# Kernel tuning notes

Hardware: AMD Instinct MI355X
Metric: run time of the kernel (lower is better)

Reference implementation:

```python
import jax, jax.numpy as jnp
import numpy as np

N_NODES = 100_000
N_EDGES = 1_600_000
IN_FEATS = 64
H_DIMS = 64
OUT_A = 2
OUT_B = 21
N_LAYERS = 2
EPS = 1e-5


def setup_inputs() -> dict:
    key = jax.random.key(0)
    ks = jax.random.split(key, 16)
    d = H_DIMS

    def rn(k, shape, scale=0.05):
        return jax.random.normal(k, shape, dtype=jnp.float32) * scale

    return {
        "v": jax.random.normal(ks[0], (N_NODES, IN_FEATS), dtype=jnp.float32),
        "src": jax.random.randint(ks[1], (N_EDGES,), 0, N_NODES),
        "dst": jax.random.randint(ks[2], (N_EDGES,), 0, N_NODES),
        "rel_type": jax.random.randint(ks[3], (N_EDGES,), 0, 3),
        "norm": jax.random.uniform(ks[4], (N_EDGES,), dtype=jnp.float32),
        "emb_W": rn(ks[5], (d, IN_FEATS)),
        "emb_b": jnp.zeros((d,), jnp.float32),
        "emb_gamma": jnp.ones((d,), jnp.float32),
        "emb_beta": jnp.zeros((d,), jnp.float32),
        "rel_weight": rn(ks[6], (3, d, d)),
        "gru_Wih": rn(ks[7], (3 * d, d)),
        "gru_Whh": rn(ks[8], (3 * d, d)),
        "gru_bih": jnp.zeros((3 * d,), jnp.float32),
        "gru_bhh": jnp.zeros((3 * d,), jnp.float32),
        "ker_gamma": jnp.ones((d,), jnp.float32),
        "ker_beta": jnp.zeros((d,), jnp.float32),
        "a_W1": rn(ks[9], (d, d)), "a_b1": jnp.zeros((d,), jnp.float32),
        "a_gamma": jnp.ones((d,), jnp.float32), "a_beta": jnp.zeros((d,), jnp.float32),
        "a_W2": rn(ks[10], (OUT_A, d)), "a_b2": jnp.zeros((OUT_A,), jnp.float32),
        "b_W1": rn(ks[11], (d, d)), "b_b1": jnp.zeros((d,), jnp.float32),
        "b_gamma": jnp.ones((d,), jnp.float32), "b_beta": jnp.zeros((d,), jnp.float32),
        "b_W2": rn(ks[12], (OUT_B, d)), "b_b2": jnp.zeros((OUT_B,), jnp.float32),
    }


def _bn(x, gamma, beta):
    # BatchNorm1d in training mode: batch statistics, biased variance
    mu = jnp.mean(x, axis=0)
    var = jnp.var(x, axis=0)
    return (x - mu) * jax.lax.rsqrt(var + EPS) * gamma + beta


def _gru_cell(x, h, Wih, Whh, bih, bhh):
    # torch nn.GRU single layer, gate order (r, z, n)
    gi = x @ Wih.T + bih
    gh = h @ Whh.T + bhh
    ir, iz, inn = jnp.split(gi, 3, axis=-1)
    hr, hz, hn = jnp.split(gh, 3, axis=-1)
    r = jax.nn.sigmoid(ir + hr)
    z = jax.nn.sigmoid(iz + hz)
    n = jnp.tanh(inn + r * hn)
    return (1.0 - z) * n + z * h


def reference(v, src, dst, rel_type, norm, emb_W, emb_b, emb_gamma, emb_beta,
              rel_weight, gru_Wih, gru_Whh, gru_bih, gru_bhh, ker_gamma, ker_beta,
              a_W1, a_b1, a_gamma, a_beta, a_W2, a_b2,
              b_W1, b_b1, b_gamma, b_beta, b_W2, b_b2):
    # Embedding: Linear -> BN -> ReLU
    h0 = jax.nn.relu(_bn(v @ emb_W.T + emb_b, emb_gamma, emb_beta))
    output = h0
    h = jnp.zeros_like(h0)
    n_nodes = v.shape[0]
    for _ in range(N_LAYERS):
        # per-node relational transform for all 3 relations: [N, 3, d]
        x3 = jnp.einsum('nd,rdk->nrk', output, rel_weight)
        msg = x3[src, rel_type] * norm[:, None]                     # [E, d]
        swh = jax.ops.segment_sum(msg, dst, num_segments=n_nodes)   # [N, d]
        h = _gru_cell(swh, h, gru_Wih, gru_Whh, gru_bih, gru_bhh)
        output = h
    hk = _bn(output, ker_gamma, ker_beta)
    # task heads: Linear -> BN -> ReLU -> Linear (MLP with h_layers=2)
    xa = jax.nn.relu(_bn(hk @ a_W1.T + a_b1, a_gamma, a_beta)) @ a_W2.T + a_b2
    xb = jax.nn.relu(_bn(hk @ b_W1.T + b_b1, b_gamma, b_beta)) @ b_W2.T + b_b2
    return xa, xb
```

## Files before the change

kernel.cpp:

```cpp
#include <hip/hip_runtime.h>

#define NN 100000
#define NE 1600000
#define NP 100096
#define NBKT 391
#define CAP 6144
#define EPSV 1e-5f

typedef unsigned int u32;
typedef unsigned short u16;
typedef unsigned long long u64;
typedef __bf16 bf16x8 __attribute__((ext_vector_type(8)));
typedef float f32x4 __attribute__((ext_vector_type(4)));

#define GLBP(x) ((const __attribute__((address_space(1))) u32*)(x))
#define LDSP(x) ((__attribute__((address_space(3))) u32*)(x))

__device__ __forceinline__ u16 f2bf(float f) {
  u32 x = __float_as_uint(f);
  return (u16)((x + 0x7FFFu + ((x >> 16) & 1u)) >> 16);
}
__device__ __forceinline__ float bf2f(u16 h) { return __uint_as_float(((u32)h) << 16); }
__device__ __forceinline__ u32 pk2(float a, float b) {
  return (u32)f2bf(a) | ((u32)f2bf(b) << 16);
}

__device__ __forceinline__ void pack_one(const float* W, u32* out, int K, int KOT, int i) {
  int q = i & 3, lane = (i >> 2) & 63, f = i >> 8;
  int ks = f / KOT, ot = f - ks * KOT;
  int o = ot * 16 + (lane & 15);
  int k = ks * 32 + (lane >> 4) * 8 + q * 2;
  out[i] = pk2(W[o * K + k], W[o * K + k + 1]);
}

__global__ void setupA(const float* __restrict__ relw, const float* __restrict__ Wih,
                       const float* __restrict__ embW, const float* __restrict__ Whh,
                       float* __restrict__ Wrow, u32* __restrict__ PWem, u32* __restrict__ PWhh) {
  int b = blockIdx.x;
  if (b < 144) {
    int t = b * 256 + threadIdx.x;
    if (t >= 192 * 192) return;
    int kg = t / 192, j = t % 192;
    const float* a = relw + (j >> 6) * 4096 + (j & 63) * 64;
    const float* w = Wih + kg * 64;
    float s = 0.f;
#pragma unroll
    for (int k = 0; k < 64; ++k) s += a[k] * w[k];
    Wrow[kg * 192 + j] = s;
  } else if (b < 152) {
    pack_one(embW, PWem, 64, 4, (b - 144) * 256 + threadIdx.x);
  } else {
    pack_one(Whh, PWhh, 64, 12, (b - 152) * 256 + threadIdx.x);
  }
}

__global__ void pack_wf(const float* __restrict__ Wrow, u32* __restrict__ PWf) {
  pack_one(Wrow, PWf, 192, 12, blockIdx.x * 256 + threadIdx.x);
}

__global__ void fold_pack(const float* __restrict__ Wa, const float* __restrict__ Wb,
                          const float* __restrict__ kacc, const float* __restrict__ kg,
                          u32* __restrict__ P) {
  int i = blockIdx.x * 256 + threadIdx.x;
  int q = i & 3, lane = (i >> 2) & 63, f = i >> 8;
  int ks = f >> 3, ot = f & 7;
  int o = ot * 16 + (lane & 15);
  int k = ks * 32 + (lane >> 4) * 8 + q * 2;
  const float* W = (o < 64) ? (Wa + o * 64) : (Wb + (o - 64) * 64);
  const float inv = 1.f / NN;
  float m0 = kacc[k] * inv;
  float s0 = kg[k] * rsqrtf(kacc[64 + k] * inv - m0 * m0 + EPSV);
  float m1 = kacc[k + 1] * inv;
  float s1 = kg[k + 1] * rsqrtf(kacc[64 + k + 1] * inv - m1 * m1 + EPSV);
  P[i] = pk2(W[k] * s0, W[k + 1] * s1);
}

__global__ __launch_bounds__(256) void countplace(const int* __restrict__ src,
                                                  const int* __restrict__ dst,
                                                  const int* __restrict__ rt,
                                                  const float* __restrict__ nrm,
                                                  int* __restrict__ gcnt,
                                                  u64* __restrict__ region) {
  __shared__ u32 hist[NBKT], gbase[NBKT];
  const int t = threadIdx.x;
  for (int i = t; i < NBKT; i += 256) hist[i] = 0;
  __syncthreads();
  const int e0 = blockIdx.x * 2048 + t;
  u32 rlo[8], rhi[8], lrank[8];
  int bkt[8];
#pragma unroll
  for (int i = 0; i < 8; ++i) {
    int e = e0 + i * 256;
    bkt[i] = -1;
    if (e < NE) {
      int d = dst[e];
      int b = d >> 8;
      bkt[i] = b;
      lrank[i] = atomicAdd(&hist[b], 1u);
      rlo[i] = (u32)src[e] | ((u32)rt[e] << 20) | ((u32)(d & 255) << 22);
      rhi[i] = __float_as_uint(nrm[e]);
    }
  }
  __syncthreads();
  for (int i = t; i < NBKT; i += 256) {
    u32 h = hist[i];
    gbase[i] = h ? (u32)atomicAdd(&gcnt[i], (int)h) : 0u;
  }
  __syncthreads();
#pragma unroll
  for (int i = 0; i < 8; ++i) {
    if (bkt[i] >= 0) {
      u32 pos = gbase[bkt[i]] + lrank[i];
      if (pos < CAP)
        region[(size_t)bkt[i] * CAP + pos] = (u64)rlo[i] | ((u64)rhi[i] << 32);
    }
  }
}

__global__ __launch_bounds__(512) void bucketscan(const int* __restrict__ gcnt,
                                                  int* __restrict__ bbase) {
  int t = threadIdx.x;
  int v = (t < NBKT) ? (gcnt[t] + 768) : 0;
  __shared__ int sh[512];
  sh[t] = v;
  __syncthreads();
#pragma unroll
  for (int off = 1; off < 512; off <<= 1) {
    int u = (t >= off) ? sh[t - off] : 0;
    __syncthreads();
    sh[t] += u;
    __syncthreads();
  }
  if (t < NBKT) bbase[t] = sh[t] - v;
}

__global__ __launch_bounds__(256) void localsort(const int* __restrict__ gcnt,
                                                 const int* __restrict__ bbase,
                                                 const u64* __restrict__ region,
                                                 u64* __restrict__ csr,
                                                 int* __restrict__ rowpr) {
  const int b = blockIdx.x, t = threadIdx.x;
  int n = gcnt[b];
  if (n > CAP) n = CAP;
  const int base = bbase[b];
  __shared__ u32 hist[1024], sc[256];
#pragma unroll
  for (int i = 0; i < 4; ++i) hist[t + 256 * i] = 0;
  __syncthreads();
  for (int i = t; i < n; i += 256)
    atomicAdd(&hist[(u32)(region[(size_t)b * CAP + i] >> 20) & 1023u], 1u);
  __syncthreads();
  u32 a0 = hist[4 * t], a1 = hist[4 * t + 1], a2 = hist[4 * t + 2];
  u32 p0 = (a0 + 1) & ~1u, p1 = (a1 + 1) & ~1u, p2 = (a2 + 1) & ~1u;
  u32 part = p0 + p1 + p2;
  sc[t] = part;
  __syncthreads();
#pragma unroll
  for (int off = 1; off < 256; off <<= 1) {
    u32 u = (t >= off) ? sc[t - off] : 0;
    __syncthreads();
    sc[t] += u;
    __syncthreads();
  }
  u32 ex = sc[t] - part;
  int node = b * 256 + t;
  rowpr[4 * node + 0] = base + (int)ex;
  rowpr[4 * node + 1] = base + (int)(ex + p0);
  rowpr[4 * node + 2] = base + (int)(ex + p0 + p1);
  rowpr[4 * node + 3] = base + (int)(ex + p0 + p1 + p2);
  __syncthreads();
  hist[4 * t + 0] = ex;
  hist[4 * t + 1] = ex + p0;
  hist[4 * t + 2] = ex + p0 + p1;
  __syncthreads();
  for (int i = t; i < n; i += 256) {
    u64 rec = region[(size_t)b * CAP + i];
    u32 pos = atomicAdd(&hist[(u32)(rec >> 20) & 1023u], 1u);
    csr[(size_t)base + pos] = rec;
  }
  __syncthreads();
  if (a0 & 1) csr[(size_t)base + ex + a0] = 0ull;
  if (a1 & 1) csr[(size_t)base + ex + p0 + a1] = 0ull;
  if (a2 & 1) csr[(size_t)base + ex + p0 + p1 + a2] = 0ull;
}

__global__ __launch_bounds__(256) void csr_gather(const int* __restrict__ rowpr,
                                                  const u64* __restrict__ csr,
                                                  const u16* __restrict__ Xbf,
                                                  u16* __restrict__ ACCbf) {
  int wv = blockIdx.x * 4 + (threadIdx.x >> 6);
  int lane = threadIdx.x & 63;
  if (wv >= NN) return;
  const int half = lane >> 5, c2 = lane & 31;
  int4 rp = *reinterpret_cast<const int4*>(rowpr + 4 * wv);
  const int b0 = __builtin_amdgcn_readfirstlane(rp.x);
  const int b1 = __builtin_amdgcn_readfirstlane(rp.y);
  const int b2 = __builtin_amdgcn_readfirstlane(rp.z);
  const int b3 = __builtin_amdgcn_readfirstlane(rp.w);
  const u32* X4 = (const u32*)Xbf;
  float a0x = 0.f, a0y = 0.f, a1x = 0.f, a1y = 0.f, a2x = 0.f, a2y = 0.f;
#define PAIRB(J, AX, AY)                                                        \
  { u32 sA = (u32)__builtin_amdgcn_readlane((int)lo, (J));                      \
    u32 sB = (u32)__builtin_amdgcn_readlane((int)lo, (J) + 1);                  \
    u32 nA = (u32)__builtin_amdgcn_readlane((int)hi, (J));                      \
    u32 nB = (u32)__builtin_amdgcn_readlane((int)hi, (J) + 1);                  \
    u32 srp = half ? sB : sA;                                                   \
    float nm = __uint_as_float(half ? nB : nA);                                 \
    u32 xw = X4[((srp & 0xFFFFFu) << 5) | (u32)c2];                             \
    AX = fmaf(__uint_as_float(xw << 16), nm, AX);                               \
    AY = fmaf(__uint_as_float(xw & 0xFFFF0000u), nm, AY); }
  for (int c = b0; c < b3; c += 64) {
    int m = b3 - c; m = m > 64 ? 64 : m;
    u32 lo = 0, hi = 0;
    if (lane < m) {
      u64 rec = csr[(size_t)c + lane];
      lo = (u32)rec; hi = (u32)(rec >> 32);
    }
    int j1 = b1 - c; j1 = j1 < 0 ? 0 : (j1 > m ? m : j1);
    int j2 = b2 - c; j2 = j2 < 0 ? 0 : (j2 > m ? m : j2);
    int j = 0;
    for (; j + 4 <= j1; j += 4) { PAIRB(j, a0x, a0y) PAIRB(j + 2, a0x, a0y) }
    if (j < j1) { PAIRB(j, a0x, a0y) j += 2; }
    for (; j + 4 <= j2; j += 4) { PAIRB(j, a1x, a1y) PAIRB(j + 2, a1x, a1y) }
    if (j < j2) { PAIRB(j, a1x, a1y) j += 2; }
    for (; j + 4 <= m; j += 4) { PAIRB(j, a2x, a2y) PAIRB(j + 2, a2x, a2y) }
    if (j < m) { PAIRB(j, a2x, a2y) j += 2; }
  }
#undef PAIRB
  a0x += __shfl_xor(a0x, 32); a0y += __shfl_xor(a0y, 32);
  a1x += __shfl_xor(a1x, 32); a1y += __shfl_xor(a1y, 32);
  a2x += __shfl_xor(a2x, 32); a2y += __shfl_xor(a2y, 32);
  if (half == 0) {
    u32* orow = (u32*)(ACCbf + (size_t)wv * 192);
    orow[c2]      = pk2(a0x, a0y);
    orow[32 + c2] = pk2(a1x, a1y);
    orow[64 + c2] = pk2(a2x, a2y);
  }
}

template<int K, int KO, int AF32, int GRU, int CS, int OUTBF>
__global__ __launch_bounds__(512) void gemm_mfma(
    const void* __restrict__ Av, const u32* __restrict__ Wpk, void* __restrict__ Yv,
    const float* __restrict__ bih, const float* __restrict__ bhh,
    const u16* __restrict__ G2B, const u16* __restrict__ Hv,
    float* __restrict__ csum, int n) {
  constexpr int KOT = KO / 16, KS = K / 32;
  constexpr int NFRAG = KS * KOT;
  __shared__ u32 bsh[NFRAG * 256];
  __shared__ float cs[2 * KO];
  const int lane = threadIdx.x & 63, w = threadIdx.x >> 6;
  const int rr = lane & 15, kg = lane >> 4;
  const long mbase = (long)blockIdx.x * 256 + w * 32;
  const u16* Abf = (const u16*)Av;
  const float* Af = (const float*)Av;

  bf16x8 abf[KS][2];
  float4 araw[AF32 ? KS : 1][2][2];
  if (AF32) {
#pragma unroll
    for (int ks = 0; ks < KS; ++ks)
#pragma unroll
      for (int hh = 0; hh < 2; ++hh) {
        long r = mbase + hh * 16 + rr;
        if (r > n - 1) r = n - 1;
        const float* pp = Af + r * K + ks * 32 + kg * 8;
        araw[ks][hh][0] = *(const float4*)pp;
        araw[ks][hh][1] = *(const float4*)(pp + 4);
      }
  } else {
#pragma unroll
    for (int ks = 0; ks < KS; ++ks)
#pragma unroll
      for (int hh = 0; hh < 2; ++hh)
        abf[ks][hh] = *reinterpret_cast<const bf16x8*>(
            Abf + (mbase + hh * 16 + rr) * K + ks * 32 + kg * 8);
  }

  constexpr int PASSES = NFRAG / 8;
#pragma unroll
  for (int i = 0; i < PASSES; ++i) {
    int c = i * 8 + w;
    __builtin_amdgcn_global_load_lds(GLBP(Wpk + (long)c * 256 + lane * 4),
                                     LDSP(&bsh[c * 256]), 16, 0, 0);
  }
  __syncthreads();

  if (AF32) {
#pragma unroll
    for (int ks = 0; ks < KS; ++ks)
#pragma unroll
      for (int hh = 0; hh < 2; ++hh) {
        float4 u0 = araw[ks][hh][0], u1 = araw[ks][hh][1];
        bf16x8 o_;
        o_[0] = __builtin_bit_cast(__bf16, f2bf(u0.x));
        o_[1] = __builtin_bit_cast(__bf16, f2bf(u0.y));
        o_[2] = __builtin_bit_cast(__bf16, f2bf(u0.z));
        o_[3] = __builtin_bit_cast(__bf16, f2bf(u0.w));
        o_[4] = __builtin_bit_cast(__bf16, f2bf(u1.x));
        o_[5] = __builtin_bit_cast(__bf16, f2bf(u1.y));
        o_[6] = __builtin_bit_cast(__bf16, f2bf(u1.z));
        o_[7] = __builtin_bit_cast(__bf16, f2bf(u1.w));
        abf[ks][hh] = o_;
      }
  }

  f32x4 acc[2][KOT] = {};
#pragma unroll
  for (int ks = 0; ks < KS; ++ks) {
#pragma unroll
    for (int o = 0; o < KOT; ++o) {
      bf16x8 bfr = *reinterpret_cast<const bf16x8*>(&bsh[((ks * KOT + o) * 64 + lane) * 4]);
      acc[0][o] = __builtin_amdgcn_mfma_f32_16x16x32_bf16(abf[ks][0], bfr, acc[0][o], 0, 0, 0);
      acc[1][o] = __builtin_amdgcn_mfma_f32_16x16x32_bf16(abf[ks][1], bfr, acc[1][o], 0, 0, 0);
    }
  }

  float s[KOT] = {}, ss[KOT] = {};
  if (GRU == 0) {
#pragma unroll
    for (int tl = 0; tl < 2; ++tl)
#pragma unroll
      for (int o = 0; o < KOT; ++o)
#pragma unroll
        for (int q = 0; q < 4; ++q) {
          long row = mbase + tl * 16 + kg * 4 + q;
          float vv = acc[tl][o][q];
          if (row < n) {
            long off = row * KO + o * 16 + rr;
            if (OUTBF) ((u16*)Yv)[off] = f2bf(vv);
            else       ((float*)Yv)[off] = vv;
            if (CS) { s[o] += vv; ss[o] += vv * vv; }
          }
        }
  } else {
    float bi[12], bh_[12];
#pragma unroll
    for (int g = 0; g < 3; ++g)
#pragma unroll
      for (int o = 0; o < 4; ++o) {
        bi[g * 4 + o] = bih[g * 64 + o * 16 + rr];
        bh_[g * 4 + o] = bhh[g * 64 + o * 16 + rr];
      }
#pragma unroll
    for (int tl = 0; tl < 2; ++tl)
#pragma unroll
      for (int o = 0; o < 4; ++o) {
        int c = o * 16 + rr;
#pragma unroll
        for (int q = 0; q < 4; ++q) {
          long row = mbase + tl * 16 + kg * 4 + q;
          float ir = acc[tl][o][q] + bi[o];
          float iz = acc[tl][o + 4][q] + bi[4 + o];
          float in_ = acc[tl][o + 8][q] + bi[8 + o];
          float hr = bh_[o], hz = bh_[4 + o], hn = bh_[8 + o], hv = 0.f;
          if (GRU == 2) {
            const u16* g2 = G2B + row * 192;
            hr += bf2f(g2[c]); hz += bf2f(g2[64 + c]); hn += bf2f(g2[128 + c]);
            hv = bf2f(Hv[row * 64 + c]);
          }
          float rg = 1.f / (1.f + __expf(-(ir + hr)));
          float zg = 1.f / (1.f + __expf(-(iz + hz)));
          float ng = tanhf(in_ + rg * hn);
          float h = (1.f - zg) * ng + (GRU == 2 ? zg * hv : 0.f);
          if (row < n) {
            ((u16*)Yv)[row * 64 + c] = f2bf(h);
            if (CS) { s[o] += h; ss[o] += h * h; }
          }
        }
      }
  }
  if (CS) {
    constexpr int LIM = (GRU == 0) ? 2 * KO : 128;
    constexpr int CKO = (GRU == 0) ? KO : 64;
    constexpr int OL = (GRU == 0) ? KOT : 4;
    for (int i = threadIdx.x; i < LIM; i += 512) cs[i] = 0.f;
    __syncthreads();
#pragma unroll
    for (int o = 0; o < OL; ++o) {
      int c = o * 16 + rr;
      atomicAdd(&cs[c], s[o]);
      atomicAdd(&cs[CKO + c], ss[o]);
    }
    __syncthreads();
    for (int i = threadIdx.x; i < LIM; i += 512) atomicAdd(&csum[i], cs[i]);
  }
}

__global__ __launch_bounds__(256) void bn_apply_bf(const float* __restrict__ X,
                                                   u16* __restrict__ Y,
                                                   const float* __restrict__ accs,
                                                   const float* __restrict__ gamma,
                                                   const float* __restrict__ beta, int relu) {
  __shared__ float scsh[128];
  int t = threadIdx.x;
  if (t < 64) {
    float mean = accs[t] * (1.f / NN);
    float var = accs[64 + t] * (1.f / NN) - mean * mean;
    float sc = gamma[t] * rsqrtf(var + EPSV);
    scsh[t] = sc;
    scsh[64 + t] = beta[t] - mean * sc;
  }
  __syncthreads();
  long i = (long)blockIdx.x * 256 + t;
  float4 v = reinterpret_cast<const float4*>(X)[i];
  int c = (int)((i * 4) & 63);
  v.x = fmaf(v.x, scsh[c],     scsh[64 + c]);
  v.y = fmaf(v.y, scsh[c + 1], scsh[65 + c]);
  v.z = fmaf(v.z, scsh[c + 2], scsh[66 + c]);
  v.w = fmaf(v.w, scsh[c + 3], scsh[67 + c]);
  if (relu) {
    v.x = fmaxf(v.x, 0.f); v.y = fmaxf(v.y, 0.f);
    v.z = fmaxf(v.z, 0.f); v.w = fmaxf(v.w, 0.f);
  }
  reinterpret_cast<ushort4*>(Y)[i] = make_ushort4(f2bf(v.x), f2bf(v.y), f2bf(v.z), f2bf(v.w));
}

template<int KO>
__global__ __launch_bounds__(256) void headfin_bn(const u16* __restrict__ Z,
                                                  const float* __restrict__ asum,
                                                  const float* __restrict__ asq,
                                                  const float* __restrict__ gamma,
                                                  const float* __restrict__ beta,
                                                  const float* __restrict__ W2,
                                                  const float* __restrict__ b2,
                                                  float* __restrict__ out, int n) {
  __shared__ float ws[KO * 64];
  __shared__ float scsh[128];
  int t = threadIdx.x;
  if (t < 64) {
    float mean = asum[t] * (1.f / NN);
    float var = asq[t] * (1.f / NN) - mean * mean;
    float sc = gamma[t] * rsqrtf(var + EPSV);
    scsh[t] = sc;
    scsh[64 + t] = beta[t] - mean * sc;
  }
  for (int i = t; i < KO * 64; i += 256) ws[i] = W2[i];
  __syncthreads();
  long node = (long)blockIdx.x * 256 + t;
  if (node >= n) return;
  const u16* zr = Z + node * 128;
  float x[64];
#pragma unroll
  for (int i = 0; i < 16; ++i) {
    ushort4 z4 = reinterpret_cast<const ushort4*>(zr)[i];
    int c = i * 4;
    x[c]     = fmaxf(fmaf(bf2f(z4.x), scsh[c],     scsh[64 + c]), 0.f);
    x[c + 1] = fmaxf(fmaf(bf2f(z4.y), scsh[c + 1], scsh[65 + c]), 0.f);
    x[c + 2] = fmaxf(fmaf(bf2f(z4.z), scsh[c + 2], scsh[66 + c]), 0.f);
    x[c + 3] = fmaxf(fmaf(bf2f(z4.w), scsh[c + 3], scsh[67 + c]), 0.f);
  }
#pragma unroll
  for (int o = 0; o < KO; ++o) {
    float a = b2[o];
#pragma unroll
    for (int d = 0; d < 64; ++d) a = fmaf(x[d], ws[o * 64 + d], a);
    out[node * KO + o] = a;
  }
}

extern "C" void kernel_launch(void* const* d_in, const int* in_sizes, int n_in,
                              void* d_out, int out_size, void* d_ws, size_t ws_size,
                              hipStream_t stream) {
  const float* v     = (const float*)d_in[0];
  const int*   src   = (const int*)d_in[1];
  const int*   dst   = (const int*)d_in[2];
  const int*   rt    = (const int*)d_in[3];
  const float* norm  = (const float*)d_in[4];
  const float* emb_W = (const float*)d_in[5];
  const float* emb_g  = (const float*)d_in[7];
  const float* emb_be = (const float*)d_in[8];
  const float* rel_w  = (const float*)d_in[9];
  const float* Wih    = (const float*)d_in[10];
  const float* Whh    = (const float*)d_in[11];
  const float* bih    = (const float*)d_in[12];
  const float* bhh    = (const float*)d_in[13];
  const float* ker_g  = (const float*)d_in[14];
  const float* aW1    = (const float*)d_in[16];
  const float* a_g  = (const float*)d_in[18];
  const float* a_be = (const float*)d_in[19];
  const float* aW2  = (const float*)d_in[20];
  const float* ab2  = (const float*)d_in[21];
  const float* bW1  = (const float*)d_in[22];
  const float* b_g  = (const float*)d_in[24];
  const float* b_be = (const float*)d_in[25];
  const float* bW2  = (const float*)d_in[26];
  const float* bb2  = (const float*)d_in[27];
  float* out = (float*)d_out;

  char* p = (char*)d_ws;
  auto nxt = [&](size_t bytes) -> char* {
    char* r = p; p += (bytes + 255) & ~(size_t)255; return r;
  };
  int*   GCNT = (int*)nxt(512 * 4);
  float* ACCs = (float*)nxt(512 * 4);
  float* Z    = (float*)nxt((size_t)NP * 64 * 4);
  u16*   X1   = (u16*)nxt((size_t)NP * 64 * 2);
  u16*   X2   = (u16*)nxt((size_t)NP * 64 * 2);
  u16*   ACCB = (u16*)nxt((size_t)NP * 192 * 2);
  u16*   G2B  = (u16*)nxt((size_t)NP * 192 * 2);
  u64*   REG  = (u64*)nxt((size_t)NBKT * CAP * 8);
  u64*   CSR  = (u64*)nxt((size_t)(NE + NBKT * 768 + 64) * 8);
  int*   BBAS = (int*)nxt(512 * 4);
  int*   ROWPR = (int*)nxt((size_t)(NP + 8) * 4 * 4);
  u32*   PWf  = (u32*)nxt(18432 * 4);
  u32*   PWem = (u32*)nxt(2048 * 4);
  u32*   PWhh = (u32*)nxt(6144 * 4);
  u32*   PWab = (u32*)nxt(4096 * 4);
  float* WROW = (float*)nxt(147456);

  hipMemsetAsync(GCNT, 0, 1024 * 4, stream);

  setupA<<<176, 256, 0, stream>>>(rel_w, Wih, emb_W, Whh, WROW, PWem, PWhh);
  countplace<<<782, 256, 0, stream>>>(src, dst, rt, norm, GCNT, REG);
  bucketscan<<<1, 512, 0, stream>>>(GCNT, BBAS);
  localsort<<<NBKT, 256, 0, stream>>>(GCNT, BBAS, REG, CSR, ROWPR);
  pack_wf<<<72, 256, 0, stream>>>(WROW, PWf);

  gemm_mfma<64, 64, 1, 0, 1, 0><<<391, 512, 0, stream>>>(v, PWem, Z, nullptr, nullptr,
                                                         nullptr, nullptr, ACCs + 0, NN);
  bn_apply_bf<<<6250, 256, 0, stream>>>(Z, X2, ACCs + 0, emb_g, emb_be, 1);

  csr_gather<<<25000, 256, 0, stream>>>(ROWPR, CSR, X2, ACCB);
  gemm_mfma<192, 192, 0, 1, 0, 1><<<391, 512, 0, stream>>>(ACCB, PWf, X1, bih, bhh,
                                                           nullptr, nullptr, nullptr, NN);

  csr_gather<<<25000, 256, 0, stream>>>(ROWPR, CSR, X1, ACCB);
  gemm_mfma<64, 192, 0, 0, 0, 1><<<391, 512, 0, stream>>>(X1, PWhh, G2B, nullptr, nullptr,
                                                          nullptr, nullptr, nullptr, NN);
  gemm_mfma<192, 192, 0, 2, 1, 1><<<391, 512, 0, stream>>>(ACCB, PWf, X1, bih, bhh,
                                                           G2B, X1, ACCs + 128, NN);

  fold_pack<<<16, 256, 0, stream>>>(aW1, bW1, ACCs + 128, ker_g, PWab);
  gemm_mfma<64, 128, 0, 0, 1, 1><<<391, 512, 0, stream>>>(X1, PWab, ACCB, nullptr, nullptr,
                                                          nullptr, nullptr, ACCs + 256, NN);
  headfin_bn<2><<<391, 256, 0, stream>>>((const u16*)ACCB, ACCs + 256, ACCs + 384,
                                         a_g, a_be, aW2, ab2, out, NN);
  headfin_bn<21><<<391, 256, 0, stream>>>((const u16*)ACCB + 64, ACCs + 320, ACCs + 448,
                                          b_g, b_be, bW2, bb2, out + (long)NN * 2, NN);
}
```

Before: 365.7 us.

## Split fused GRU GEMM into per-gate GEMM blocks plus separate combine kernel

Replaces the monolithic GRU GEMM kernels, which computed all 192 gate outputs per block and applied the nonlinearity in the epilogue, with a gate_gemm that launches one grid slice per gate (r, z, n_input, and n_hidden in layer 2). Layer 2 concatenates the Whh term into the K dimension for the r and z gates. A separate elementwise gru_combine kernel then applies the sigmoid/tanh update and accumulates BN statistics. The aim is more parallel blocks, lower register pressure and less LDS per block, and removal of the separate Whh GEMM. The cost is an extra bf16 round-trip of gate pre-activations through global memory, an extra kernel launch per layer, and bf16 rounding of the pre-activations. Workspace buffers are aliased to make room for the gate outputs.

```diff
diff --git a/kernel.cpp b/kernel.cpp
--- a/kernel.cpp
+++ b/kernel.cpp
@@ -24,6 +24,7 @@
 __device__ __forceinline__ u32 pk2(float a, float b) {
   return (u32)f2bf(a) | ((u32)f2bf(b) << 16);
 }
+__device__ __forceinline__ float sigm(float x) { return 1.f / (1.f + __expf(-x)); }
 
 __device__ __forceinline__ void pack_one(const float* W, u32* out, int K, int KOT, int i) {
   int q = i & 3, lane = (i >> 2) & 63, f = i >> 8;
@@ -34,8 +35,8 @@
 }
 
 __global__ void setupA(const float* __restrict__ relw, const float* __restrict__ Wih,
-                       const float* __restrict__ embW, const float* __restrict__ Whh,
-                       float* __restrict__ Wrow, u32* __restrict__ PWem, u32* __restrict__ PWhh) {
+                       const float* __restrict__ embW,
+                       float* __restrict__ Wrow, u32* __restrict__ PWem) {
   int b = blockIdx.x;
   if (b < 144) {
     int t = b * 256 + threadIdx.x;
@@ -47,15 +48,43 @@
 #pragma unroll
     for (int k = 0; k < 64; ++k) s += a[k] * w[k];
     Wrow[kg * 192 + j] = s;
-  } else if (b < 152) {
+  } else {
     pack_one(embW, PWem, 64, 4, (b - 144) * 256 + threadIdx.x);
+  }
+}
+
+__global__ void pack_g1(const float* __restrict__ Wrow, u32* __restrict__ P) {
+  int i = blockIdx.x * 256 + threadIdx.x;
+  int q = i & 3, lane = (i >> 2) & 63, f = i >> 8;
+  int g = f / 24, fl = f - g * 24;
+  int ks = fl >> 2, o = fl & 3;
+  int row = g * 64 + o * 16 + (lane & 15);
+  int k = ks * 32 + (lane >> 4) * 8 + q * 2;
+  P[i] = pk2(Wrow[row * 192 + k], Wrow[row * 192 + k + 1]);
+}
+
+__global__ void pack_g2(const float* __restrict__ Wrow, const float* __restrict__ Whh,
+                        u32* __restrict__ P) {
+  int i = blockIdx.x * 256 + threadIdx.x;
+  int q = i & 3, lane = (i >> 2) & 63, f = i >> 8;
+  int g = f >> 5, fl = f & 31;
+  int ks = fl >> 2, o = fl & 3;
+  u32 val = 0u;
+  if (ks < 6) {
+    if (g < 3) {
+      int row = g * 64 + o * 16 + (lane & 15);
+      int k = ks * 32 + (lane >> 4) * 8 + q * 2;
+      val = pk2(Wrow[row * 192 + k], Wrow[row * 192 + k + 1]);
+    }
   } else {
-    pack_one(Whh, PWhh, 64, 12, (b - 152) * 256 + threadIdx.x);
-  }
-}
-
-__global__ void pack_wf(const float* __restrict__ Wrow, u32* __restrict__ PWf) {
-  pack_one(Wrow, PWf, 192, 12, blockIdx.x * 256 + threadIdx.x);
+    int g2 = (g < 2) ? g : (g == 3 ? 2 : -1);
+    if (g2 >= 0) {
+      int row = g2 * 64 + o * 16 + (lane & 15);
+      int k = (ks - 6) * 32 + (lane >> 4) * 8 + q * 2;
+      val = pk2(Whh[row * 64 + k], Whh[row * 64 + k + 1]);
+    }
+  }
+  P[i] = val;
 }
 
 __global__ void fold_pack(const float* __restrict__ Wa, const float* __restrict__ Wb,
@@ -238,11 +267,124 @@
   }
 }
 
-template<int K, int KO, int AF32, int GRU, int CS, int OUTBF>
+template<int LAYER>
+__global__ __launch_bounds__(512, 6) void gate_gemm(
+    const u16* __restrict__ A1, const u16* __restrict__ A2,
+    const u32* __restrict__ Pg, u16* __restrict__ GG, int n) {
+  constexpr int KSP = (LAYER == 1) ? 6 : 8;
+  constexpr int NFRAG = KSP * 4;
+  __shared__ u32 bsh[NFRAG * 256];
+  const int g = blockIdx.x / NBKT, blk = blockIdx.x - g * NBKT;
+  int ksl = 0, ksh = 6;
+  if (LAYER == 2) { ksl = (g == 3) ? 6 : 0; ksh = (g == 2) ? 6 : 8; }
+  const int lane = threadIdx.x & 63, w = threadIdx.x >> 6;
+  const int rr = lane & 15, kg = lane >> 4;
+  const long mbase = (long)blk * 256 + w * 32;
+
+  const u32* P = Pg + (long)g * NFRAG * 256;
+#pragma unroll
+  for (int i = 0; i < NFRAG / 8; ++i) {
+    int c = i * 8 + w;
+    __builtin_amdgcn_global_load_lds(GLBP(P + (long)c * 256 + lane * 4),
+                                     LDSP(&bsh[c * 256]), 16, 0, 0);
+  }
+  __syncthreads();
+
+  f32x4 acc[2][4] = {};
+  for (int ks = ksl; ks < ksh; ++ks) {
+    bf16x8 a0, a1;
+    if (ks < 6) {
+      a0 = *reinterpret_cast<const bf16x8*>(A1 + (mbase + rr) * 192 + ks * 32 + kg * 8);
+      a1 = *reinterpret_cast<const bf16x8*>(A1 + (mbase + 16 + rr) * 192 + ks * 32 + kg * 8);
+    } else {
+      a0 = *reinterpret_cast<const bf16x8*>(A2 + (mbase + rr) * 64 + (ks - 6) * 32 + kg * 8);
+      a1 = *reinterpret_cast<const bf16x8*>(A2 + (mbase + 16 + rr) * 64 + (ks - 6) * 32 + kg * 8);
+    }
+#pragma unroll
+    for (int o = 0; o < 4; ++o) {
+      bf16x8 b = *reinterpret_cast<const bf16x8*>(&bsh[((ks * 4 + o) * 64 + lane) * 4]);
+      acc[0][o] = __builtin_amdgcn_mfma_f32_16x16x32_bf16(a0, b, acc[0][o], 0, 0, 0);
+      acc[1][o] = __builtin_amdgcn_mfma_f32_16x16x32_bf16(a1, b, acc[1][o], 0, 0, 0);
+    }
+  }
+
+  u16* Gg = GG + (long)g * ((long)NP * 64);
+#pragma unroll
+  for (int tl = 0; tl < 2; ++tl)
+#pragma unroll
+    for (int o = 0; o < 4; ++o)
+#pragma unroll
+      for (int q = 0; q < 4; ++q) {
+        long row = mbase + tl * 16 + kg * 4 + q;
+        if (row < n) Gg[row * 64 + o * 16 + rr] = f2bf(acc[tl][o][q]);
+      }
+}
+
+template<int USE_H, int CS>
+__global__ __launch_bounds__(256) void gru_combine(
+    const u16* __restrict__ GG, const u16* __restrict__ Hin, u16* __restrict__ Hout,
+    const float* __restrict__ bih, const float* __restrict__ bhh,
+    float* __restrict__ csum) {
+  __shared__ float cs[128];
+  const int t = threadIdx.x;
+  if (CS) {
+    for (int i = t; i < 128; i += 256) cs[i] = 0.f;
+    __syncthreads();
+  }
+  float s[4] = {0.f, 0.f, 0.f, 0.f}, ss[4] = {0.f, 0.f, 0.f, 0.f};
+  const long tot = (long)NN * 16;
+  int c0 = -1;
+  for (long i = (long)blockIdx.x * 256 + t; i < tot; i += (long)gridDim.x * 256) {
+    long node = i >> 4;
+    c0 = (int)(i & 15) * 4;
+    ushort4 vr = *reinterpret_cast<const ushort4*>(GG + node * 64 + c0);
+    ushort4 vz = *reinterpret_cast<const ushort4*>(GG + (long)NP * 64 + node * 64 + c0);
+    ushort4 vi = *reinterpret_cast<const ushort4*>(GG + (long)2 * NP * 64 + node * 64 + c0);
+    ushort4 vh = make_ushort4(0, 0, 0, 0), hv = make_ushort4(0, 0, 0, 0);
+    if (USE_H) {
+      vh = *reinterpret_cast<const ushort4*>(GG + (long)3 * NP * 64 + node * 64 + c0);
+      hv = *reinterpret_cast<const ushort4*>(Hin + node * 64 + c0);
+    }
+    u16 gr[4] = {vr.x, vr.y, vr.z, vr.w};
+    u16 gz[4] = {vz.x, vz.y, vz.z, vz.w};
+    u16 gi[4] = {vi.x, vi.y, vi.z, vi.w};
+    u16 gh[4] = {vh.x, vh.y, vh.z, vh.w};
+    u16 hl[4] = {hv.x, hv.y, hv.z, hv.w};
+    u16 ov[4];
+#pragma unroll
+    for (int k = 0; k < 4; ++k) {
+      int c = c0 + k;
+      float r = sigm(bf2f(gr[k]) + bih[c] + bhh[c]);
+      float z = sigm(bf2f(gz[k]) + bih[64 + c] + bhh[64 + c]);
+      float h;
+      if (USE_H) {
+        float ng = tanhf(bf2f(gi[k]) + bih[128 + c] + r * (bf2f(gh[k]) + bhh[128 + c]));
+        h = (1.f - z) * ng + z * bf2f(hl[k]);
+      } else {
+        float ng = tanhf(bf2f(gi[k]) + bih[128 + c] + r * bhh[128 + c]);
+        h = (1.f - z) * ng;
+      }
+      ov[k] = f2bf(h);
+      if (CS) { s[k] += h; ss[k] += h * h; }
+    }
+    *reinterpret_cast<ushort4*>(Hout + node * 64 + c0) = make_ushort4(ov[0], ov[1], ov[2], ov[3]);
+  }
+  if (CS) {
+    if (c0 >= 0) {
+#pragma unroll
+      for (int k = 0; k < 4; ++k) {
+        atomicAdd(&cs[c0 + k], s[k]);
+        atomicAdd(&cs[64 + c0 + k], ss[k]);
+      }
+    }
+    __syncthreads();
+    if (t < 128) atomicAdd(&csum[t], cs[t]);
+  }
+}
+
+template<int K, int KO, int AF32, int CS, int OUTBF>
 __global__ __launch_bounds__(512) void gemm_mfma(
     const void* __restrict__ Av, const u32* __restrict__ Wpk, void* __restrict__ Yv,
-    const float* __restrict__ bih, const float* __restrict__ bhh,
-    const u16* __restrict__ G2B, const u16* __restrict__ Hv,
     float* __restrict__ csum, int n) {
   constexpr int KOT = KO / 16, KS = K / 32;
   constexpr int NFRAG = KS * KOT;
@@ -316,73 +458,32 @@
   }
 
   float s[KOT] = {}, ss[KOT] = {};
-  if (GRU == 0) {
-#pragma unroll
-    for (int tl = 0; tl < 2; ++tl)
-#pragma unroll
-      for (int o = 0; o < KOT; ++o)
-#pragma unroll
-        for (int q = 0; q < 4; ++q) {
-          long row = mbase + tl * 16 + kg * 4 + q;
-          float vv = acc[tl][o][q];
-          if (row < n) {
-            long off = row * KO + o * 16 + rr;
-            if (OUTBF) ((u16*)Yv)[off] = f2bf(vv);
-            else       ((float*)Yv)[off] = vv;
-            if (CS) { s[o] += vv; ss[o] += vv * vv; }
-          }
-        }
-  } else {
-    float bi[12], bh_[12];
-#pragma unroll
-    for (int g = 0; g < 3; ++g)
-#pragma unroll
-      for (int o = 0; o < 4; ++o) {
-        bi[g * 4 + o] = bih[g * 64 + o * 16 + rr];
-        bh_[g * 4 + o] = bhh[g * 64 + o * 16 + rr];
-      }
-#pragma unroll
-    for (int tl = 0; tl < 2; ++tl)
-#pragma unroll
-      for (int o = 0; o < 4; ++o) {
-        int c = o * 16 + rr;
-#pragma unroll
-        for (int q = 0; q < 4; ++q) {
-          long row = mbase + tl * 16 + kg * 4 + q;
-          float ir = acc[tl][o][q] + bi[o];
-          float iz = acc[tl][o + 4][q] + bi[4 + o];
-          float in_ = acc[tl][o + 8][q] + bi[8 + o];
-          float hr = bh_[o], hz = bh_[4 + o], hn = bh_[8 + o], hv = 0.f;
-          if (GRU == 2) {
-            const u16* g2 = G2B + row * 192;
-            hr += bf2f(g2[c]); hz += bf2f(g2[64 + c]); hn += bf2f(g2[128 + c]);
-            hv = bf2f(Hv[row * 64 + c]);
-          }
-          float rg = 1.f / (1.f + __expf(-(ir + hr)));
-          float zg = 1.f / (1.f + __expf(-(iz + hz)));
-          float ng = tanhf(in_ + rg * hn);
-          float h = (1.f - zg) * ng + (GRU == 2 ? zg * hv : 0.f);
-          if (row < n) {
-            ((u16*)Yv)[row * 64 + c] = f2bf(h);
-            if (CS) { s[o] += h; ss[o] += h * h; }
-          }
+#pragma unroll
+  for (int tl = 0; tl < 2; ++tl)
+#pragma unroll
+    for (int o = 0; o < KOT; ++o)
+#pragma unroll
+      for (int q = 0; q < 4; ++q) {
+        long row = mbase + tl * 16 + kg * 4 + q;
+        float vv = acc[tl][o][q];
+        if (row < n) {
+          long off = row * KO + o * 16 + rr;
+          if (OUTBF) ((u16*)Yv)[off] = f2bf(vv);
+          else       ((float*)Yv)[off] = vv;
+          if (CS) { s[o] += vv; ss[o] += vv * vv; }
         }
       }
-  }
   if (CS) {
-    constexpr int LIM = (GRU == 0) ? 2 * KO : 128;
-    constexpr int CKO = (GRU == 0) ? KO : 64;
-    constexpr int OL = (GRU == 0) ? KOT : 4;
-    for (int i = threadIdx.x; i < LIM; i += 512) cs[i] = 0.f;
-    __syncthreads();
-#pragma unroll
-    for (int o = 0; o < OL; ++o) {
+    for (int i = threadIdx.x; i < 2 * KO; i += 512) cs[i] = 0.f;
+    __syncthreads();
+#pragma unroll
+    for (int o = 0; o < KOT; ++o) {
       int c = o * 16 + rr;
       atomicAdd(&cs[c], s[o]);
-      atomicAdd(&cs[CKO + c], ss[o]);
-    }
-    __syncthreads();
-    for (int i = threadIdx.x; i < LIM; i += 512) atomicAdd(&csum[i], cs[i]);
+      atomicAdd(&cs[KO + c], ss[o]);
+    }
+    __syncthreads();
+    for (int i = threadIdx.x; i < 2 * KO; i += 512) atomicAdd(&csum[i], cs[i]);
   }
 }
 
@@ -493,46 +594,44 @@
   };
   int*   GCNT = (int*)nxt(512 * 4);
   float* ACCs = (float*)nxt(512 * 4);
-  float* Z    = (float*)nxt((size_t)NP * 64 * 4);
+  char*  GGZ  = nxt((size_t)NP * 64 * 4 + (size_t)NP * 64 * 2 + (size_t)NBKT * CAP * 8);
+  float* Z    = (float*)GGZ;
+  u16*   X2   = (u16*)(GGZ + (size_t)NP * 64 * 4);
+  u64*   REG  = (u64*)(GGZ + (size_t)NP * 64 * 4 + (size_t)NP * 64 * 2);
+  u16*   GG   = (u16*)GGZ;
   u16*   X1   = (u16*)nxt((size_t)NP * 64 * 2);
-  u16*   X2   = (u16*)nxt((size_t)NP * 64 * 2);
   u16*   ACCB = (u16*)nxt((size_t)NP * 192 * 2);
-  u16*   G2B  = (u16*)nxt((size_t)NP * 192 * 2);
-  u64*   REG  = (u64*)nxt((size_t)NBKT * CAP * 8);
   u64*   CSR  = (u64*)nxt((size_t)(NE + NBKT * 768 + 64) * 8);
   int*   BBAS = (int*)nxt(512 * 4);
   int*   ROWPR = (int*)nxt((size_t)(NP + 8) * 4 * 4);
-  u32*   PWf  = (u32*)nxt(18432 * 4);
   u32*   PWem = (u32*)nxt(2048 * 4);
-  u32*   PWhh = (u32*)nxt(6144 * 4);
+  u32*   PG1  = (u32*)nxt(18432 * 4);
+  u32*   PG2  = (u32*)nxt(32768 * 4);
   u32*   PWab = (u32*)nxt(4096 * 4);
   float* WROW = (float*)nxt(147456);
 
   hipMemsetAsync(GCNT, 0, 1024 * 4, stream);
 
-  setupA<<<176, 256, 0, stream>>>(rel_w, Wih, emb_W, Whh, WROW, PWem, PWhh);
+  setupA<<<152, 256, 0, stream>>>(rel_w, Wih, emb_W, WROW, PWem);
   countplace<<<782, 256, 0, stream>>>(src, dst, rt, norm, GCNT, REG);
   bucketscan<<<1, 512, 0, stream>>>(GCNT, BBAS);
   localsort<<<NBKT, 256, 0, stream>>>(GCNT, BBAS, REG, CSR, ROWPR);
-  pack_wf<<<72, 256, 0, stream>>>(WROW, PWf);
-
-  gemm_mfma<64, 64, 1, 0, 1, 0><<<391, 512, 0, stream>>>(v, PWem, Z, nullptr, nullptr,
-                                                         nullptr, nullptr, ACCs + 0, NN);
+  pack_g1<<<72, 256, 0, stream>>>(WROW, PG1);
+  pack_g2<<<128, 256, 0, stream>>>(WROW, Whh, PG2);
+
+  gemm_mfma<64, 64, 1, 1, 0><<<391, 512, 0, stream>>>(v, PWem, Z, ACCs + 0, NN);
   bn_apply_bf<<<6250, 256, 0, stream>>>(Z, X2, ACCs + 0, emb_g, emb_be, 1);
 
   csr_gather<<<25000, 256, 0, stream>>>(ROWPR, CSR, X2, ACCB);
-  gemm_mfma<192, 192, 0, 1, 0, 1><<<391, 512, 0, stream>>>(ACCB, PWf, X1, bih, bhh,
-                                                           nullptr, nullptr, nullptr, NN);
+  gate_gemm<1><<<3 * NBKT, 512, 0, stream>>>(ACCB, (const u16*)nullptr, PG1, GG, NN);
+  gru_combine<0, 0><<<6250, 256, 0, stream>>>(GG, (const u16*)nullptr, X1, bih, bhh, nullptr);
 
   csr_gather<<<25000, 256, 0, stream>>>(ROWPR, CSR, X1, ACCB);
-  gemm_mfma<64, 192, 0, 0, 0, 1><<<391, 512, 0, stream>>>(X1, PWhh, G2B, nullptr, nullptr,
-                                                          nullptr, nullptr, nullptr, NN);
-  gemm_mfma<192, 192, 0, 2, 1, 1><<<391, 512, 0, stream>>>(ACCB, PWf, X1, bih, bhh,
-                                                           G2B, X1, ACCs + 128, NN);
+  gate_gemm<2><<<4 * NBKT, 512, 0, stream>>>(ACCB, X1, PG2, GG, NN);
+  gru_combine<1, 1><<<416, 256, 0, stream>>>(GG, X1, X1, bih, bhh, ACCs + 128);
 
   fold_pack<<<16, 256, 0, stream>>>(aW1, bW1, ACCs + 128, ker_g, PWab);
-  gemm_mfma<64, 128, 0, 0, 1, 1><<<391, 512, 0, stream>>>(X1, PWab, ACCB, nullptr, nullptr,
-                                                          nullptr, nullptr, ACCs + 256, NN);
+  gemm_mfma<64, 128, 0, 1, 1><<<391, 512, 0, stream>>>(X1, PWab, ACCB, ACCs + 256, NN);
   headfin_bn<2><<<391, 256, 0, stream>>>((const u16*)ACCB, ACCs + 256, ACCs + 384,
                                          a_g, a_be, aW2, ab2, out, NN);
   headfin_bn<21><<<391, 256, 0, stream>>>((const u16*)ACCB + 64, ACCs + 320, ACCs + 448,
```

Result: slower. 424.1 us (+16.0%).
